# Performance work log

Hardware: AMD Instinct MI355X
Metric: run time of the kernel (lower is better)

Reference implementation:

```python
import jax, jax.numpy as jnp
import numpy as np

D_MODEL = 1024
NUM_HEADS = 16
D_K = D_MODEL // NUM_HEADS
B, S = 4, 2048


def setup_inputs() -> dict:
    key = jax.random.key(0)
    ks = jax.random.split(key, 11)
    scale = 1.0 / np.sqrt(D_MODEL)
    inp = {
        "query": jax.random.normal(ks[0], (B, S, D_MODEL), jnp.float32),
        "key_": jax.random.normal(ks[1], (B, S, D_MODEL), jnp.float32),
        "value": jax.random.normal(ks[2], (B, S, D_MODEL), jnp.float32),
        "w_q": jax.random.normal(ks[3], (D_MODEL, D_MODEL), jnp.float32) * scale,
        "b_q": jnp.zeros((D_MODEL,), jnp.float32),
        "w_k": jax.random.normal(ks[4], (D_MODEL, D_MODEL), jnp.float32) * scale,
        "b_k": jnp.zeros((D_MODEL,), jnp.float32),
        "w_v": jax.random.normal(ks[5], (D_MODEL, D_MODEL), jnp.float32) * scale,
        "b_v": jnp.zeros((D_MODEL,), jnp.float32),
        "w_o": jax.random.normal(ks[6], (D_MODEL, D_MODEL), jnp.float32) * scale,
        "b_o": jnp.zeros((D_MODEL,), jnp.float32),
    }
    return inp


def _split_heads(x):
    b, s, _ = x.shape
    return x.reshape(b, s, NUM_HEADS, D_K).transpose(0, 2, 1, 3)  # [b,h,s,dk]


def reference(query, key_, value, w_q, b_q, w_k, b_k, w_v, b_v, w_o, b_o):
    # Linear layers: y = x @ W^T + b (torch nn.Linear convention, W is [out,in])
    Q = _split_heads(query @ w_q.T + b_q)
    K = _split_heads(key_ @ w_k.T + b_k)
    V = _split_heads(value @ w_v.T + b_v)
    scores = jnp.einsum("bhqd,bhkd->bhqk", Q, K) / jnp.sqrt(jnp.float32(D_K))
    probs = jax.nn.softmax(scores, axis=-1)
    attn = jnp.einsum("bhqk,bhkd->bhqd", probs, V)  # [b,h,s,dk]
    attn = attn.transpose(0, 2, 1, 3).reshape(query.shape[0], query.shape[1], D_MODEL)
    return attn @ w_o.T + b_o
```

## Files before the change

### kernel.cpp

```cpp
#include <hip/hip_runtime.h>
#include <hip/hip_bf16.h>
#include <math.h>

#define DM   1024
#define NH   16
#define DKH  64
#define BB   4
#define SS   2048
#define MT   8192

#define QSCALE 0.18033688011112042f

typedef short bf16x8 __attribute__((ext_vector_type(8)));
typedef float f32x4  __attribute__((ext_vector_type(4)));
typedef float f32x16 __attribute__((ext_vector_type(16)));

__device__ __forceinline__ unsigned short f2bf(float f) {
  union { float f; unsigned u; } a; a.f = f;
  unsigned r = (a.u + 0x7fffu + ((a.u >> 16) & 1u)) >> 16;
  return (unsigned short)r;
}

__device__ __forceinline__ void load_lds16(const void* g, void* l) {
  __builtin_amdgcn_global_load_lds(
      (const __attribute__((address_space(1))) void*)g,
      (__attribute__((address_space(3))) void*)l, 16, 0, 0);
}

__global__ void cvt_all(const float* __restrict__ q, const float* __restrict__ k,
                        const float* __restrict__ v, const float* __restrict__ wq,
                        const float* __restrict__ wk, const float* __restrict__ wv,
                        const float* __restrict__ wo,
                        unsigned short* __restrict__ xq, unsigned short* __restrict__ xk,
                        unsigned short* __restrict__ xv, unsigned short* __restrict__ uwq,
                        unsigned short* __restrict__ uwk, unsigned short* __restrict__ uwv,
                        unsigned short* __restrict__ uwo) {
  const long NQ = (long)MT * DM / 4;
  const long NW = (long)DM * DM / 4;
  const long total = 3 * NQ + 4 * NW;
  for (long i = (long)blockIdx.x * blockDim.x + threadIdx.x; i < total;
       i += (long)gridDim.x * blockDim.x) {
    const float* s; unsigned short* d; long o;
    if      (i <     NQ)          { s = q;  d = xq;  o = i; }
    else if (i < 2 * NQ)          { s = k;  d = xk;  o = i - NQ; }
    else if (i < 3 * NQ)          { s = v;  d = xv;  o = i - 2 * NQ; }
    else if (i < 3 * NQ + NW)     { s = wq; d = uwq; o = i - 3 * NQ; }
    else if (i < 3 * NQ + 2 * NW) { s = wk; d = uwk; o = i - 3 * NQ - NW; }
    else if (i < 3 * NQ + 3 * NW) { s = wv; d = uwv; o = i - 3 * NQ - 2 * NW; }
    else                          { s = wo; d = uwo; o = i - 3 * NQ - 3 * NW; }
    float4 f = ((const float4*)s)[o];
    ushort4 u;
    u.x = f2bf(f.x); u.y = f2bf(f.y); u.z = f2bf(f.z); u.w = f2bf(f.w);
    ((ushort4*)d)[o] = u;
  }
}

template <int MODE>
__global__ __launch_bounds__(256, 2)
void gemm_bt(const unsigned short* __restrict__ X, const unsigned short* __restrict__ Wt,
             const float* __restrict__ bias, float oscale, void* __restrict__ Y) {
  __shared__ __align__(16) unsigned short Al[128 * 64];
  __shared__ __align__(16) unsigned short Bl[128 * 64];
  const int t = threadIdx.x, lane = t & 63, w = t >> 6;
  const int wr = w >> 1, wc = w & 1;
  const int m0 = blockIdx.y * 128, n0 = blockIdx.x * 128;
  const int lr = lane & 15, lk8 = (lane >> 4) * 8;

  f32x4 acc[4][4] = {};

  for (int kt = 0; kt < 16; ++kt) {
    const int k0 = kt * 64;
#pragma unroll
    for (int p = 0; p < 4; ++p) {
      const int row = (t >> 3) + 32 * p, c8 = (t & 7) * 8;
      load_lds16(X  + (size_t)(m0 + row) * DM + k0 + c8, &Al[row * 64 + c8]);
      load_lds16(Wt + (size_t)(n0 + row) * DM + k0 + c8, &Bl[row * 64 + c8]);
    }
    asm volatile("s_waitcnt vmcnt(0)" ::: "memory");
    __syncthreads();
#pragma unroll
    for (int kk = 0; kk < 2; ++kk) {
      bf16x8 af[4], bfr[4];
#pragma unroll
      for (int m = 0; m < 4; ++m)
        af[m] = *(const bf16x8*)&Al[(64 * wr + 16 * m + lr) * 64 + kk * 32 + lk8];
#pragma unroll
      for (int n = 0; n < 4; ++n)
        bfr[n] = *(const bf16x8*)&Bl[(64 * wc + 16 * n + lr) * 64 + kk * 32 + lk8];
#pragma unroll
      for (int m = 0; m < 4; ++m)
#pragma unroll
        for (int n = 0; n < 4; ++n)
          acc[m][n] = __builtin_amdgcn_mfma_f32_16x16x32_bf16(af[m], bfr[n], acc[m][n], 0, 0, 0);
    }
    __syncthreads();
  }

#pragma unroll
  for (int m = 0; m < 4; ++m)
#pragma unroll
    for (int n = 0; n < 4; ++n)
#pragma unroll
      for (int j = 0; j < 4; ++j) {
        const int row = m0 + 64 * wr + 16 * m + (lane >> 4) * 4 + j;
        const int col = n0 + 64 * wc + 16 * n + lr;
        const float val = (acc[m][n][j] + bias[col]) * oscale;
        if (MODE == 0) {
          const int b = row >> 11, s = row & 2047, h = col >> 6, dk = col & 63;
          ((unsigned short*)Y)[(((size_t)(b * NH + h)) * SS + s) * DKH + dk] = f2bf(val);
        } else {
          ((float*)Y)[(size_t)row * DM + col] = val;
        }
      }
}

__global__ __launch_bounds__(256)
void transposeV(const unsigned short* __restrict__ VH, unsigned short* __restrict__ VTg) {
  __shared__ unsigned short T[64][66];
  const int t = threadIdx.x;
  const int bh = blockIdx.y, s0 = blockIdx.x * 64;
  const unsigned short* src = VH + ((size_t)bh * SS + s0) * DKH;
#pragma unroll
  for (int p = 0; p < 2; ++p) {
    const int c = p * 256 + t, row = c >> 3, c8 = (c & 7) * 8;
    bf16x8 v = *(const bf16x8*)(src + (size_t)row * DKH + c8);
#pragma unroll
    for (int e = 0; e < 8; ++e) T[row][c8 + e] = (unsigned short)v[e];
  }
  __syncthreads();
#pragma unroll
  for (int p = 0; p < 2; ++p) {
    const int c = p * 256 + t, dk = c >> 3, s8 = (c & 7) * 8;
    bf16x8 v;
#pragma unroll
    for (int e = 0; e < 8; ++e) v[e] = (short)T[s8 + e][dk];
    *(bf16x8*)(VTg + ((size_t)bh * DKH + dk) * SS + s0 + s8) = v;
  }
}

__global__ __launch_bounds__(512, 4)
void attn(const unsigned short* __restrict__ Qh, const unsigned short* __restrict__ Kh,
          const unsigned short* __restrict__ VTg, unsigned short* __restrict__ Ctx) {
  __shared__ __align__(16) unsigned short Kl[2][4096];
  __shared__ __align__(16) unsigned short Vl[2][4096];

  const int t = threadIdx.x, lane = t & 63, w = t >> 6;
  const int lr32 = lane & 31, hi = lane >> 5;
  const int bh = blockIdx.y;
  const int q0 = blockIdx.x * 256;
  const unsigned short* Qp = Qh + (size_t)bh * SS * DKH;
  const unsigned short* Kp = Kh + (size_t)bh * SS * DKH;
  const unsigned short* Vp = VTg + (size_t)bh * DKH * SS;

  const int qrow = q0 + w * 32 + lr32;
  bf16x8 qB[4];
#pragma unroll
  for (int ks = 0; ks < 4; ++ks)
    qB[ks] = *(const bf16x8*)(Qp + (size_t)qrow * DKH + 16 * ks + 8 * hi);

  f32x16 accO[2] = {};
  float m = -INFINITY, l = 0.f;

  const int srow = t >> 3;
  const int scol = (((t & 7) * 16) ^ ((srow & 7) << 4)) >> 1;

#define STAGE(kt_, buf_)                                                      \
  {                                                                           \
    load_lds16(Kp + (size_t)((kt_) * 64 + srow) * DKH + scol,                 \
               &Kl[buf_][t * 8]);                                             \
    load_lds16(Vp + (size_t)srow * SS + (kt_) * 64 + scol,                    \
               &Vl[buf_][t * 8]);                                             \
  }

  STAGE(0, 0);
  asm volatile("s_waitcnt vmcnt(0)" ::: "memory");
  __syncthreads();

  const int rsw = (lr32 & 7) << 4;
  int obase[4];
#pragma unroll
  for (int j = 0; j < 4; ++j)
    obase[j] = lr32 * 128 + ((32 * j + 16 * hi) ^ rsw);

  for (int kt = 0; kt < 32; ++kt) {
    const int buf = kt & 1;
    if (kt + 1 < 32) STAGE(kt + 1, buf ^ 1);

    const char* Kbase = (const char*)&Kl[buf][0];
    const char* Vbase = (const char*)&Vl[buf][0];

#pragma unroll
    for (int kb = 0; kb < 2; ++kb) {
      f32x16 s = {};
      __builtin_amdgcn_s_setprio(1);
#pragma unroll
      for (int ks = 0; ks < 4; ++ks) {
        bf16x8 ka = *(const bf16x8*)(Kbase + kb * 4096 + obase[ks]);
        s = __builtin_amdgcn_mfma_f32_32x32x16_bf16(ka, qB[ks], s, 0, 0, 0);
      }
      __builtin_amdgcn_s_setprio(0);

      float m0 = fmaxf(fmaxf(s[0], s[1]), fmaxf(s[2], s[3]));
      float m1 = fmaxf(fmaxf(s[4], s[5]), fmaxf(s[6], s[7]));
      float m2 = fmaxf(fmaxf(s[8], s[9]), fmaxf(s[10], s[11]));
      float m3 = fmaxf(fmaxf(s[12], s[13]), fmaxf(s[14], s[15]));
      float pmax = fmaxf(fmaxf(m0, m1), fmaxf(m2, m3));
      pmax = fmaxf(pmax, __shfl_xor(pmax, 32));

      if (!__all(pmax - m <= 8.0f)) {
        const float mnew = fmaxf(m, pmax);
        const float al = __builtin_amdgcn_exp2f(m - mnew);
        l *= al;
        const int abase = hi * 16;
#pragma unroll
        for (int r = 0; r < 16; ++r) {
          const int rho4 = ((r & 3) + 8 * (r >> 2)) * 4;
          const float ar = __int_as_float(
              __builtin_amdgcn_ds_bpermute(abase + rho4, __float_as_int(al)));
          accO[0][r] *= ar;
          accO[1][r] *= ar;
        }
        m = mnew;
      }

#pragma unroll
      for (int r = 0; r < 16; ++r) s[r] = __builtin_amdgcn_exp2f(s[r] - m);
      float s0 = (s[0] + s[1]) + (s[2] + s[3]);
      float s1 = (s[4] + s[5]) + (s[6] + s[7]);
      float s2 = (s[8] + s[9]) + (s[10] + s[11]);
      float s3 = (s[12] + s[13]) + (s[14] + s[15]);
      float ps = (s0 + s1) + (s2 + s3);
      ps += __shfl_xor(ps, 32);
      l += ps;

      unsigned W[8];
#pragma unroll
      for (int g = 0; g < 4; ++g) {
        asm("v_cvt_pk_bf16_f32 %0, %1, %2" : "=v"(W[2 * g])     : "v"(s[4 * g]),     "v"(s[4 * g + 1]));
        asm("v_cvt_pk_bf16_f32 %0, %1, %2" : "=v"(W[2 * g + 1]) : "v"(s[4 * g + 2]), "v"(s[4 * g + 3]));
      }

#pragma unroll
      for (int cl = 0; cl < 2; ++cl) {
        auto r0 = __builtin_amdgcn_permlane32_swap(W[4 * cl],     W[4 * cl + 2], false, false);
        auto r1 = __builtin_amdgcn_permlane32_swap(W[4 * cl + 1], W[4 * cl + 3], false, false);
        union { unsigned u[4]; bf16x8 v; } pa;
        pa.u[0] = r0[0]; pa.u[1] = r1[0]; pa.u[2] = r0[1]; pa.u[3] = r1[1];
        __builtin_amdgcn_s_setprio(1);
#pragma unroll
        for (int dblk = 0; dblk < 2; ++dblk) {
          bf16x8 vb = *(const bf16x8*)(Vbase + dblk * 4096 + obase[2 * kb + cl]);
          accO[dblk] = __builtin_amdgcn_mfma_f32_32x32x16_bf16(pa.v, vb, accO[dblk], 0, 0, 0);
        }
        __builtin_amdgcn_s_setprio(0);
      }
    }

    asm volatile("s_waitcnt vmcnt(0)" ::: "memory");
    __syncthreads();
  }

  const float inv = 1.f / l;
  const int b = bh >> 4, h = bh & 15;
  const int abase = hi * 16;
#pragma unroll
  for (int r = 0; r < 16; ++r) {
    const int rho = (r & 3) + 8 * (r >> 2) + 4 * hi;
    const float invr = __int_as_float(
        __builtin_amdgcn_ds_bpermute(abase + ((r & 3) + 8 * (r >> 2)) * 4, __float_as_int(inv)));
    const int token = b * SS + q0 + w * 32 + rho;
#pragma unroll
    for (int dblk = 0; dblk < 2; ++dblk)
      Ctx[(size_t)token * DM + h * DKH + 32 * dblk + lr32] = f2bf(accO[dblk][r] * invr);
  }
}

extern "C" void kernel_launch(void* const* d_in, const int* in_sizes, int n_in,
                              void* d_out, int out_size, void* d_ws, size_t ws_size,
                              hipStream_t stream) {
  const float* q  = (const float*)d_in[0];
  const float* k  = (const float*)d_in[1];
  const float* v  = (const float*)d_in[2];
  const float* wq = (const float*)d_in[3];
  const float* bq = (const float*)d_in[4];
  const float* wk = (const float*)d_in[5];
  const float* bk = (const float*)d_in[6];
  const float* wv = (const float*)d_in[7];
  const float* bv = (const float*)d_in[8];
  const float* wo = (const float*)d_in[9];
  const float* bo = (const float*)d_in[10];

  char* ws = (char*)d_ws;
  const size_t ACT = (size_t)MT * DM * 2;
  const size_t WSZ = (size_t)DM * DM * 2;
  unsigned short* XQ  = (unsigned short*)(ws);
  unsigned short* XK  = (unsigned short*)(ws + ACT);
  unsigned short* XV  = (unsigned short*)(ws + 2 * ACT);
  unsigned short* WQb = (unsigned short*)(ws + 3 * ACT);
  unsigned short* WKb = (unsigned short*)(ws + 3 * ACT + WSZ);
  unsigned short* WVb = (unsigned short*)(ws + 3 * ACT + 2 * WSZ);
  unsigned short* WOb = (unsigned short*)(ws + 3 * ACT + 3 * WSZ);
  unsigned short* QH  = (unsigned short*)(ws + 3 * ACT + 4 * WSZ);
  unsigned short* KH  = (unsigned short*)(ws + 4 * ACT + 4 * WSZ);
  unsigned short* VH  = (unsigned short*)(ws + 5 * ACT + 4 * WSZ);
  unsigned short* CTX = (unsigned short*)(ws + 6 * ACT + 4 * WSZ);
  unsigned short* VT  = XQ;

  cvt_all<<<dim3(2048), dim3(256), 0, stream>>>(q, k, v, wq, wk, wv, wo,
                                                XQ, XK, XV, WQb, WKb, WVb, WOb);

  const dim3 gg(DM / 128, MT / 128, 1);
  gemm_bt<0><<<gg, 256, 0, stream>>>(XQ, WQb, bq, QSCALE, QH);
  gemm_bt<0><<<gg, 256, 0, stream>>>(XK, WKb, bk, 1.0f, KH);
  gemm_bt<0><<<gg, 256, 0, stream>>>(XV, WVb, bv, 1.0f, VH);

  transposeV<<<dim3(SS / 64, BB * NH), 256, 0, stream>>>(VH, VT);

  attn<<<dim3(SS / 256, BB * NH), 512, 0, stream>>>(QH, KH, VT, CTX);

  gemm_bt<1><<<gg, 256, 0, stream>>>(CTX, WOb, bo, 1.0f, (float*)d_out);
}
```

Before: 382.6 us.

## Double-buffer swizzled GEMM with 256-row tiles and batch QKV projections in one launch

```diff
diff --git a/kernel.cpp b/kernel.cpp
--- a/kernel.cpp
+++ b/kernel.cpp
@@ -56,62 +56,102 @@
 }
 
 template <int MODE>
-__global__ __launch_bounds__(256, 2)
-void gemm_bt(const unsigned short* __restrict__ X, const unsigned short* __restrict__ Wt,
-             const float* __restrict__ bias, float oscale, void* __restrict__ Y) {
-  __shared__ __align__(16) unsigned short Al[128 * 64];
-  __shared__ __align__(16) unsigned short Bl[128 * 64];
+__global__ __launch_bounds__(512, 2)
+void gemm2ph(const unsigned short* __restrict__ Xb, const unsigned short* __restrict__ Wb,
+             const float* __restrict__ bz0, const float* __restrict__ bz1,
+             const float* __restrict__ bz2, float oscale0, void* __restrict__ Yb) {
+  __shared__ __align__(16) unsigned short Al[2][256 * 64];
+  __shared__ __align__(16) unsigned short Bl[2][128 * 64];
+
   const int t = threadIdx.x, lane = t & 63, w = t >> 6;
-  const int wr = w >> 1, wc = w & 1;
-  const int m0 = blockIdx.y * 128, n0 = blockIdx.x * 128;
-  const int lr = lane & 15, lk8 = (lane >> 4) * 8;
+  const int wm = w >> 1, wn = w & 1;
+  const int z = blockIdx.z;
+  const unsigned short* X  = Xb + (size_t)z * MT * DM;
+  const unsigned short* Wt = Wb + (size_t)z * DM * DM;
+  const float* bias = (z == 0) ? bz0 : (z == 1 ? bz1 : bz2);
+  const float osc = (z == 0) ? oscale0 : 1.0f;
+  const int m0 = blockIdx.y * 256, n0 = blockIdx.x * 128;
+  const int lr = lane & 15, lg = lane >> 4;
 
   f32x4 acc[4][4] = {};
 
+  int srow[4], scol[4];
+#pragma unroll
+  for (int p = 0; p < 4; ++p) {
+    const int c = t + 512 * p;
+    srow[p] = c >> 3;
+    scol[p] = (((c & 7) * 16) ^ ((srow[p] & 7) << 4)) >> 1;
+  }
+
+#define GSTAGE(kt_, buf_)                                                     \
+  {                                                                           \
+    _Pragma("unroll")                                                         \
+    for (int p = 0; p < 4; ++p)                                               \
+      load_lds16(X + (size_t)(m0 + srow[p]) * DM + (kt_) * 64 + scol[p],      \
+                 &Al[buf_][(t + 512 * p) * 8]);                               \
+    _Pragma("unroll")                                                         \
+    for (int p = 0; p < 2; ++p)                                               \
+      load_lds16(Wt + (size_t)(n0 + srow[p]) * DM + (kt_) * 64 + scol[p],     \
+                 &Bl[buf_][(t + 512 * p) * 8]);                               \
+  }
+
+  GSTAGE(0, 0);
+  asm volatile("s_waitcnt vmcnt(0)" ::: "memory");
+  __syncthreads();
+
+  const int rsw = (lr & 7) << 4;
+  int aoff[4][2], boff[4][2];
+#pragma unroll
+  for (int f = 0; f < 4; ++f)
+#pragma unroll
+    for (int kk = 0; kk < 2; ++kk) {
+      aoff[f][kk] = (wm * 64 + f * 16 + lr) * 128 + ((kk * 64 + lg * 16) ^ rsw);
+      boff[f][kk] = (wn * 64 + f * 16 + lr) * 128 + ((kk * 64 + lg * 16) ^ rsw);
+    }
+
   for (int kt = 0; kt < 16; ++kt) {
-    const int k0 = kt * 64;
-#pragma unroll
-    for (int p = 0; p < 4; ++p) {
-      const int row = (t >> 3) + 32 * p, c8 = (t & 7) * 8;
-      load_lds16(X  + (size_t)(m0 + row) * DM + k0 + c8, &Al[row * 64 + c8]);
-      load_lds16(Wt + (size_t)(n0 + row) * DM + k0 + c8, &Bl[row * 64 + c8]);
+    const int buf = kt & 1;
+    if (kt + 1 < 16) GSTAGE(kt + 1, buf ^ 1);
+
+    const char* Ab = (const char*)&Al[buf][0];
+    const char* Bb = (const char*)&Bl[buf][0];
+#pragma unroll
+    for (int kk = 0; kk < 2; ++kk) {
+      bf16x8 af[4], bfv[4];
+#pragma unroll
+      for (int mf = 0; mf < 4; ++mf) af[mf] = *(const bf16x8*)(Ab + aoff[mf][kk]);
+#pragma unroll
+      for (int nf = 0; nf < 4; ++nf) bfv[nf] = *(const bf16x8*)(Bb + boff[nf][kk]);
+#pragma unroll
+      for (int mf = 0; mf < 4; ++mf)
+#pragma unroll
+        for (int nf = 0; nf < 4; ++nf)
+          acc[mf][nf] = __builtin_amdgcn_mfma_f32_16x16x32_bf16(af[mf], bfv[nf], acc[mf][nf], 0, 0, 0);
     }
+
     asm volatile("s_waitcnt vmcnt(0)" ::: "memory");
     __syncthreads();
-#pragma unroll
-    for (int kk = 0; kk < 2; ++kk) {
-      bf16x8 af[4], bfr[4];
-#pragma unroll
-      for (int m = 0; m < 4; ++m)
-        af[m] = *(const bf16x8*)&Al[(64 * wr + 16 * m + lr) * 64 + kk * 32 + lk8];
-#pragma unroll
-      for (int n = 0; n < 4; ++n)
-        bfr[n] = *(const bf16x8*)&Bl[(64 * wc + 16 * n + lr) * 64 + kk * 32 + lk8];
-#pragma unroll
-      for (int m = 0; m < 4; ++m)
-#pragma unroll
-        for (int n = 0; n < 4; ++n)
-          acc[m][n] = __builtin_amdgcn_mfma_f32_16x16x32_bf16(af[m], bfr[n], acc[m][n], 0, 0, 0);
-    }
-    __syncthreads();
-  }
-
-#pragma unroll
-  for (int m = 0; m < 4; ++m)
-#pragma unroll
-    for (int n = 0; n < 4; ++n)
+  }
+
+#pragma unroll
+  for (int mf = 0; mf < 4; ++mf)
+#pragma unroll
+    for (int nf = 0; nf < 4; ++nf) {
+      const int col = n0 + wn * 64 + nf * 16 + lr;
+      const float bcol = bias[col];
 #pragma unroll
       for (int j = 0; j < 4; ++j) {
-        const int row = m0 + 64 * wr + 16 * m + (lane >> 4) * 4 + j;
-        const int col = n0 + 64 * wc + 16 * n + lr;
-        const float val = (acc[m][n][j] + bias[col]) * oscale;
+        const int row = m0 + wm * 64 + mf * 16 + lg * 4 + j;
+        const float val = (acc[mf][nf][j] + bcol) * osc;
         if (MODE == 0) {
           const int b = row >> 11, s = row & 2047, h = col >> 6, dk = col & 63;
-          ((unsigned short*)Y)[(((size_t)(b * NH + h)) * SS + s) * DKH + dk] = f2bf(val);
+          ((unsigned short*)Yb)[(size_t)z * MT * DM +
+              (((size_t)(b * NH + h)) * SS + s) * DKH + dk] = f2bf(val);
         } else {
-          ((float*)Y)[(size_t)row * DM + col] = val;
+          ((float*)Yb)[(size_t)row * DM + col] = val;
         }
       }
+    }
 }
 
 __global__ __launch_bounds__(256)
@@ -309,14 +349,13 @@
   cvt_all<<<dim3(2048), dim3(256), 0, stream>>>(q, k, v, wq, wk, wv, wo,
                                                 XQ, XK, XV, WQb, WKb, WVb, WOb);
 
-  const dim3 gg(DM / 128, MT / 128, 1);
-  gemm_bt<0><<<gg, 256, 0, stream>>>(XQ, WQb, bq, QSCALE, QH);
-  gemm_bt<0><<<gg, 256, 0, stream>>>(XK, WKb, bk, 1.0f, KH);
-  gemm_bt<0><<<gg, 256, 0, stream>>>(XV, WVb, bv, 1.0f, VH);
+  gemm2ph<0><<<dim3(DM / 128, MT / 256, 3), 512, 0, stream>>>(
+      XQ, WQb, bq, bk, bv, QSCALE, QH);
 
   transposeV<<<dim3(SS / 64, BB * NH), 256, 0, stream>>>(VH, VT);
 
   attn<<<dim3(SS / 256, BB * NH), 512, 0, stream>>>(QH, KH, VT, CTX);
 
-  gemm_bt<1><<<gg, 256, 0, stream>>>(CTX, WOb, bo, 1.0f, (float*)d_out);
-}
+  gemm2ph<1><<<dim3(DM / 128, MT / 256, 1), 512, 0, stream>>>(
+      CTX, WOb, bo, bo, bo, 1.0f, (float*)d_out);
+}
```

Result: slower. 402.7 us (+5.2%).
